# Performance work log

Hardware: AMD Instinct MI355X
Metric: run time of the kernel (lower is better)

Reference implementation:

```python
import jax, jax.numpy as jnp
import numpy as np

B = 8388608
AGE_MAX = 120.0
INV_SQRT_PI = 1.0 / np.sqrt(np.pi).astype(np.float32)
INV_SQRT_2PI = 1.0 / np.sqrt(2.0 * np.pi).astype(np.float32)


def _ndtr(z):
    # standard normal CDF via erf
    return 0.5 * (1.0 + jax.lax.erf(z * np.float32(1.0 / np.sqrt(2.0))))


def _I_norm(mu, sigma2, y):
    # Faithful translation of CRPS.I_norm (closed-form CRPS of Normal(mu, s) at y)
    s = jnp.sqrt(sigma2)
    ystd = (y - mu) / s
    ncdf = _ndtr(ystd)                              # Normal(mu,s).cdf(y)
    npdf = jnp.exp(-0.5 * ystd * ystd) * INV_SQRT_2PI / s  # Normal(mu,s).pdf(y)
    n2cdf = _ndtr(ystd * np.float32(np.sqrt(2.0)))  # Normal(mu, s/sqrt(2)).cdf(y)
    return s * (ystd * ncdf * ncdf + 2.0 * ncdf * npdf * s - INV_SQRT_PI * n2cdf)


def setup_inputs() -> dict:
    key = jax.random.key(0)
    k1, k2, k3 = jax.random.split(key, 3)
    pred_params = jax.random.normal(k1, (B, 2), dtype=jnp.float32)  # [mu, log_sigma2]
    tgts = jax.random.uniform(k2, (B, 2), dtype=jnp.float32, minval=1e-3, maxval=1.0)  # [tte, censor]
    ages = jax.random.uniform(k3, (B,), dtype=jnp.float32, minval=0.0, maxval=1.0)
    return {"pred_params": pred_params, "tgts": tgts, "ages": ages, "use_intvl": 1}


def reference(pred_params, tgts, ages, use_intvl):
    mu = pred_params[:, 0]
    sigma2 = jnp.exp(pred_params[:, 1])  # s.exp() in original
    tte = tgts[:, 0]
    censor = tgts[:, 1]
    max_tte = AGE_MAX - ages
    Y = jnp.log(tte)       # time.log() / log(e)
    T = jnp.log(max_tte)

    I = lambda y: _I_norm(mu, sigma2, y)
    I_ = lambda y: _I_norm(-mu, sigma2, y)

    if use_intvl:
        crps = I(Y) + I_(-T) + (1.0 - censor) * (I_(-Y) - I_(-T))
    else:
        crps = I(Y) + (1.0 - censor) * I_(-Y)
    return jnp.sum(crps) / np.float32(B)
```

## Files before the change

kernel.cpp:

```cpp
#include <hip/hip_runtime.h>
#include <math.h>


#define AGE_MAX_F     120.0f
#define INV_SQRT_PI_F 0.5641895835477563f
#define INV_SQRT_2PI_F 0.3989422804014327f
#define INV_SQRT_2_F  0.7071067811865476f
#define SQRT_2_F      1.4142135623730951f
#define B_TOTAL       8388608.0f

__device__ __forceinline__ float ndtr_f(float z) {
    return 0.5f * (1.0f + erff(z * INV_SQRT_2_F));
}

__global__ __launch_bounds__(256) void crps_kernel(
    const float4* __restrict__ pp,
    const float4* __restrict__ tg,
    const float2* __restrict__ ag,
    const int*    __restrict__ use_intvl_p,
    float*        __restrict__ out,
    int npairs, float inv_total)
{
    const int tid    = blockIdx.x * blockDim.x + threadIdx.x;
    const int stride = gridDim.x * blockDim.x;
    const int use_intvl = *use_intvl_p;

    float acc = 0.0f;

    for (int i = tid; i < npairs; i += stride) {
        const float4 p = pp[i];
        const float4 t = tg[i];
        const float2 a = ag[i];

        #pragma unroll
        for (int j = 0; j < 2; ++j) {
            const float mu  = j ? p.z : p.x;
            const float ls  = j ? p.w : p.y;
            const float tte = j ? t.z : t.x;
            const float cen = j ? t.w : t.y;
            const float age = j ? a.y : a.x;

            const float s     = __expf( 0.5f * ls);
            const float inv_s = __expf(-0.5f * ls);
            const float Y     = __logf(tte);

            const float dy  = Y - mu;
            const float z   = dy * inv_s;
            const float c   = ndtr_f(z);
            const float pdf = __expf(-0.5f * z * z) * INV_SQRT_2PI_F;
            const float c2  = ndtr_f(z * SQRT_2_F);

            const float IY  =  dy * c * c
                             + 2.0f * s * c * pdf
                             - s * INV_SQRT_PI_F * c2;
            const float omc  = 1.0f - c;
            const float omc2 = 1.0f - c2;
            const float InY  = -dy * omc * omc
                             + 2.0f * s * omc * pdf
                             - s * INV_SQRT_PI_F * omc2;

            float crps;
            if (use_intvl) {
                const float T   = __logf(AGE_MAX_F - age);
                const float dt  = mu - T;
                const float zt  = dt * inv_s;
                const float ct  = ndtr_f(zt);
                const float pt  = __expf(-0.5f * zt * zt) * INV_SQRT_2PI_F;
                const float c2t = ndtr_f(zt * SQRT_2_F);
                const float InT =  dt * ct * ct
                                 + 2.0f * s * ct * pt
                                 - s * INV_SQRT_PI_F * c2t;
                crps = IY + InT + (1.0f - cen) * (InY - InT);
            } else {
                crps = IY + (1.0f - cen) * InY;
            }
            acc += crps;
        }
    }

    #pragma unroll
    for (int off = 32; off > 0; off >>= 1)
        acc += __shfl_down(acc, off);

    __shared__ float wsum[4];
    const int lane = threadIdx.x & 63;
    const int wid  = threadIdx.x >> 6;
    if (lane == 0) wsum[wid] = acc;
    __syncthreads();
    if (threadIdx.x == 0) {
        const float blocksum = wsum[0] + wsum[1] + wsum[2] + wsum[3];
        atomicAdd(out, blocksum * inv_total);
    }
}

extern "C" void kernel_launch(void* const* d_in, const int* in_sizes, int n_in,
                              void* d_out, int out_size, void* d_ws, size_t ws_size,
                              hipStream_t stream) {
    const float4* pp = (const float4*)d_in[0];
    const float4* tg = (const float4*)d_in[1];
    const float2* ag = (const float2*)d_in[2];
    const int*    ui = (const int*)d_in[3];
    float* out = (float*)d_out;

    const int n      = in_sizes[2];
    const int npairs = n >> 1;
    const float inv_total = 1.0f / (float)n;

    hipMemsetAsync(d_out, 0, sizeof(float), stream);

    int blocks = (npairs + 255) / 256;
    if (blocks > 2048) blocks = 2048;
    crps_kernel<<<blocks, 256, 0, stream>>>(pp, tg, ag, ui, out, npairs, inv_total);
}
```

Before: 189.0 us.

## Replace erf with polynomial normal CDF reusing pdf, unroll grid loop by two

Replaces the erff-based normal CDF with an Abramowitz-Stegun style rational polynomial that reuses the already-computed Gaussian pdf. The pdf for the sqrt(2)-scaled argument is derived by squaring the existing pdf, which avoids an extra exp. The grid-stride loop is also unrolled by two so more loads are in flight at once. The polynomial approximation has about 1e-7 absolute error, so it lowers accuracy slightly in exchange for fewer transcendental and ALU instructions.

After: 181.9 us. -3.8%, faster.

```diff
diff --git a/kernel.cpp b/kernel.cpp
--- a/kernel.cpp
+++ b/kernel.cpp
@@ -2,15 +2,60 @@
 #include <math.h>
 
 
-#define AGE_MAX_F     120.0f
-#define INV_SQRT_PI_F 0.5641895835477563f
+#define AGE_MAX_F      120.0f
+#define INV_SQRT_PI_F  0.5641895835477563f
 #define INV_SQRT_2PI_F 0.3989422804014327f
-#define INV_SQRT_2_F  0.7071067811865476f
-#define SQRT_2_F      1.4142135623730951f
-#define B_TOTAL       8388608.0f
+#define SQRT_2PI_F     2.5066282746310002f
+#define SQRT_2_F       1.4142135623730951f
 
-__device__ __forceinline__ float ndtr_f(float z) {
-    return 0.5f * (1.0f + erff(z * INV_SQRT_2_F));
+__device__ __forceinline__ float ndtr_from_pdf(float z, float phi) {
+    const float za = fabsf(z);
+    const float t  = __builtin_amdgcn_rcpf(fmaf(0.2316419f, za, 1.0f));
+    float p = fmaf(1.330274429f, t, -1.821255978f);
+    p = fmaf(p, t, 1.781477937f);
+    p = fmaf(p, t, -0.356563782f);
+    p = fmaf(p, t, 0.319381530f);
+    p = p * t;
+    const float hm = fmaf(-phi, p, 0.5f);
+    return fmaf(copysignf(1.0f, z), hm, 0.5f);
+}
+
+__device__ __forceinline__ float crps_elem(float mu, float ls, float tte,
+                                           float cen, float age, int use_intvl) {
+    const float s     = __expf( 0.5f * ls);
+    const float inv_s = __expf(-0.5f * ls);
+    const float Y     = __logf(tte);
+
+    const float dy  = Y - mu;
+    const float z   = dy * inv_s;
+    const float pdf = __expf(-0.5f * z * z) * INV_SQRT_2PI_F;
+    const float c   = ndtr_from_pdf(z, pdf);
+    const float pdf2 = pdf * pdf * SQRT_2PI_F;
+    const float c2  = ndtr_from_pdf(z * SQRT_2_F, pdf2);
+
+    const float sp  = s * INV_SQRT_PI_F;
+    const float IY  = dy * c * c + 2.0f * s * c * pdf - sp * c2;
+    const float omc = 1.0f - c;
+    const float InY = -dy * omc * omc + 2.0f * s * omc * pdf - sp * (1.0f - c2);
+
+    if (use_intvl) {
+        const float T    = __logf(AGE_MAX_F - age);
+        const float dt   = mu - T;
+        const float zt   = dt * inv_s;
+        const float pdft = __expf(-0.5f * zt * zt) * INV_SQRT_2PI_F;
+        const float ct   = ndtr_from_pdf(zt, pdft);
+        const float pdft2 = pdft * pdft * SQRT_2PI_F;
+        const float c2t  = ndtr_from_pdf(zt * SQRT_2_F, pdft2);
+        const float InT  = dt * ct * ct + 2.0f * s * ct * pdft - sp * c2t;
+        return IY + InT + (1.0f - cen) * (InY - InT);
+    } else {
+        return IY + (1.0f - cen) * InY;
+    }
+}
+
+__device__ __forceinline__ float crps_pair(float4 p, float4 t, float2 a, int ui) {
+    return crps_elem(p.x, p.y, t.x, t.y, a.x, ui)
+         + crps_elem(p.z, p.w, t.z, t.w, a.y, ui);
 }
 
 __global__ __launch_bounds__(256) void crps_kernel(
@@ -23,59 +68,23 @@
 {
     const int tid    = blockIdx.x * blockDim.x + threadIdx.x;
     const int stride = gridDim.x * blockDim.x;
-    const int use_intvl = *use_intvl_p;
+    const int ui     = *use_intvl_p;
 
     float acc = 0.0f;
 
-    for (int i = tid; i < npairs; i += stride) {
-        const float4 p = pp[i];
-        const float4 t = tg[i];
-        const float2 a = ag[i];
-
-        #pragma unroll
-        for (int j = 0; j < 2; ++j) {
-            const float mu  = j ? p.z : p.x;
-            const float ls  = j ? p.w : p.y;
-            const float tte = j ? t.z : t.x;
-            const float cen = j ? t.w : t.y;
-            const float age = j ? a.y : a.x;
-
-            const float s     = __expf( 0.5f * ls);
-            const float inv_s = __expf(-0.5f * ls);
-            const float Y     = __logf(tte);
-
-            const float dy  = Y - mu;
-            const float z   = dy * inv_s;
-            const float c   = ndtr_f(z);
-            const float pdf = __expf(-0.5f * z * z) * INV_SQRT_2PI_F;
-            const float c2  = ndtr_f(z * SQRT_2_F);
-
-            const float IY  =  dy * c * c
-                             + 2.0f * s * c * pdf
-                             - s * INV_SQRT_PI_F * c2;
-            const float omc  = 1.0f - c;
-            const float omc2 = 1.0f - c2;
-            const float InY  = -dy * omc * omc
-                             + 2.0f * s * omc * pdf
-                             - s * INV_SQRT_PI_F * omc2;
-
-            float crps;
-            if (use_intvl) {
-                const float T   = __logf(AGE_MAX_F - age);
-                const float dt  = mu - T;
-                const float zt  = dt * inv_s;
-                const float ct  = ndtr_f(zt);
-                const float pt  = __expf(-0.5f * zt * zt) * INV_SQRT_2PI_F;
-                const float c2t = ndtr_f(zt * SQRT_2_F);
-                const float InT =  dt * ct * ct
-                                 + 2.0f * s * ct * pt
-                                 - s * INV_SQRT_PI_F * c2t;
-                crps = IY + InT + (1.0f - cen) * (InY - InT);
-            } else {
-                crps = IY + (1.0f - cen) * InY;
-            }
-            acc += crps;
-        }
+    int i = tid;
+    for (; i + stride < npairs; i += 2 * stride) {
+        const float4 p0 = pp[i];
+        const float4 t0 = tg[i];
+        const float2 a0 = ag[i];
+        const float4 p1 = pp[i + stride];
+        const float4 t1 = tg[i + stride];
+        const float2 a1 = ag[i + stride];
+        acc += crps_pair(p0, t0, a0, ui);
+        acc += crps_pair(p1, t1, a1, ui);
+    }
+    for (; i < npairs; i += stride) {
+        acc += crps_pair(pp[i], tg[i], ag[i], ui);
     }
 
     #pragma unroll
```
